# Kernel optimization log

Measured on AMD Instinct MI355X. Metric: run time of the kernel, lower is better.

The kernel has to match this reference:

```python
import jax, jax.numpy as jnp
import numpy as np

B, L, LATENT, HID, NTOK = 65536, 8, 256, 128, 5


def setup_inputs() -> dict:
    key = jax.random.key(0)
    ks = jax.random.split(key, 8)
    s = 0.05  # small init scale for stable GRU dynamics
    return {
        "latent_context": jax.random.normal(ks[0], (B, LATENT), jnp.float32),
        "target_sequence": jax.random.randint(ks[1], (B, L), 0, NTOK),
        "emb_table": jax.random.normal(ks[2], (NTOK + 1, HID), jnp.float32) * s,
        "W_ih": jax.random.normal(ks[3], (3 * LATENT, HID), jnp.float32) * s,
        "W_hh": jax.random.normal(ks[4], (3 * LATENT, LATENT), jnp.float32) * s,
        "b_ih": jnp.zeros((3 * LATENT,), jnp.float32),
        "b_hh": jnp.zeros((3 * LATENT,), jnp.float32),
        "W_out": jax.random.normal(ks[5], (NTOK, LATENT), jnp.float32) * s,
        "b_out": jnp.zeros((NTOK,), jnp.float32),
    }


def reference(latent_context, target_sequence, emb_table, W_ih, W_hh, b_ih, b_hh, W_out, b_out):
    b = latent_context.shape[0]
    start_idx = emb_table.shape[0] - 1  # start token index = num_tokens
    # Teacher forcing: input token at step 0 is <start>, then target[:, :-1]
    tokens = jnp.concatenate(
        [jnp.full((b, 1), start_idx, dtype=target_sequence.dtype), target_sequence[:, :-1]],
        axis=1,
    )  # (B, L)
    emb = emb_table[tokens]  # (B, L, HID) embedding gather, done once

    def gru_step(h, x):
        # x: (B, HID), h: (B, LATENT). PyTorch GRU cell math.
        gi = x @ W_ih.T + b_ih          # (B, 3*LATENT)
        gh = h @ W_hh.T + b_hh          # (B, 3*LATENT)
        i_r, i_z, i_n = jnp.split(gi, 3, axis=-1)
        h_r, h_z, h_n = jnp.split(gh, 3, axis=-1)
        r = jax.nn.sigmoid(i_r + h_r)
        z = jax.nn.sigmoid(i_z + h_z)
        n = jnp.tanh(i_n + r * h_n)
        h_new = (1.0 - z) * n + z * h
        step_logits = h_new @ W_out.T + b_out  # (B, NTOK)
        return h_new, step_logits

    _, logits = jax.lax.scan(gru_step, latent_context, jnp.swapaxes(emb, 0, 1))
    return jnp.swapaxes(logits, 0, 1)  # (B, L, NTOK)
```

## Files before the change

kernel.cpp:

```cpp
#include <hip/hip_runtime.h>
#include <hip/hip_bf16.h>


typedef __attribute__((ext_vector_type(8)))  __bf16 bf16x8;
typedef __attribute__((ext_vector_type(4)))  __bf16 bf16x4;
typedef __attribute__((ext_vector_type(8)))  unsigned short u16x8;
typedef __attribute__((ext_vector_type(4)))  float  f32x4;

#define LOG2E_F     1.4426950408889634f
#define TWO_LOG2E_F 2.8853900817779268f

#if __has_builtin(__builtin_amdgcn_exp2f)
#define EXP2F(x) __builtin_amdgcn_exp2f(x)
#else
#define EXP2F(x) __expf((x) * 0.6931471805599453f)
#endif

__device__ __forceinline__ float sigm2(float a) {
    return __builtin_amdgcn_rcpf(1.f + EXP2F(-a));
}
__device__ __forceinline__ float tanh2(float a) {
    return __builtin_fmaf(2.f, __builtin_amdgcn_rcpf(1.f + EXP2F(-a)), -1.f);
}
__device__ __forceinline__ void lds_barrier() {
    __builtin_amdgcn_sched_barrier(0);
    asm volatile("s_waitcnt lgkmcnt(0)" ::: "memory");
    __builtin_amdgcn_s_barrier();
    __builtin_amdgcn_sched_barrier(0);
}

#define MFMA16(a, b, c) __builtin_amdgcn_mfma_f32_16x16x32_bf16((a), (b), (c), 0, 0, 0)

__global__ void k_gtable(const float* __restrict__ emb, const float* __restrict__ W_ih,
                         const float* __restrict__ b_ih, const float* __restrict__ b_hh,
                         float* __restrict__ G) {
    int tok = blockIdx.x;
    int j   = threadIdx.x;
    const float4* e4 = (const float4*)(emb + tok * 128);
    const float4* w4 = (const float4*)(W_ih + (size_t)j * 128);
    float s = 0.f;
#pragma unroll
    for (int k = 0; k < 32; ++k) {
        float4 a = e4[k], b = w4[k];
        s += a.x * b.x + a.y * b.y + a.z * b.z + a.w * b.w;
    }
    s += b_ih[j];
    if (j < 512) s = (s + b_hh[j]) * LOG2E_F;
    else         s = s * TWO_LOG2E_F;
    G[tok * 768 + j] = s;
}

__global__ void k_wfrag3(const float* __restrict__ Whh, const float* __restrict__ Gtab,
                         const float* __restrict__ b_hh, __bf16* __restrict__ Wg) {
    int u    = blockIdx.x * 256 + threadIdx.x;
    int lane = u & 63;
    int frag = u >> 6;
    int w    = frag / 28;
    int f    = frag - 28 * w;
    int col  = w * 16 + (lane & 15);
    int kq   = lane >> 4;
    bf16x8 v;
    if (f < 24) {
        int g = f >> 3, kc = f & 7;
        float scale = (g < 2) ? LOG2E_F : TWO_LOG2E_F;
        const float* src = Whh + (size_t)(g * 256 + col) * 256 + kc * 32 + kq * 8;
#pragma unroll
        for (int j = 0; j < 8; ++j) v[j] = (__bf16)(src[j] * scale);
    } else {
        int g = f - 24;
#pragma unroll
        for (int j = 0; j < 8; ++j) {
            int k = kq * 8 + j;
            float val = 0.f;
            if (k < 6) {
                val = (g == 0) ? Gtab[k * 768 + col]
                    : (g == 1) ? Gtab[k * 768 + 256 + col]
                    : (g == 2) ? b_hh[512 + col] * TWO_LOG2E_F
                               : Gtab[k * 768 + 512 + col];
            }
            v[j] = (__bf16)val;
        }
    }
    *(bf16x8*)(Wg + (size_t)u * 8) = v;
}

__global__ __launch_bounds__(1024) void k_main(
    const float* __restrict__ latent, const int* __restrict__ tgt,
    const __bf16* __restrict__ Wg, const float* __restrict__ Wout,
    const float* __restrict__ bout, float* __restrict__ out) {

    __shared__ __bf16 h_lds[2][4][8][64][8];
    __shared__ __bf16 ohc_lds[8][4][16][8];
    __shared__ __bf16 wstage_lds[16][4][64][8];
    __shared__ __bf16 woutf_lds[8][64][8];
    __shared__ float  logit_lds[64 * 40];

    const int tid  = threadIdx.x;
    const int lane = tid & 63;
    const int w    = tid >> 6;
    const int q    = lane >> 4;
    const int n16  = lane & 15;
    const int row0 = blockIdx.x * 64;

    const __bf16* wbase = Wg + ((size_t)(w * 28) * 64 + lane) * 8;

    const int kc_h  = w >> 1;
    const int slotl = n16 + 16 * ((2 * w + (q >> 1)) & 3);
    const int joff  = 4 * (q & 1);

    if (tid < 512) {
        int kc = tid >> 6, ln = tid & 63, m = ln & 15, kq2 = ln >> 4;
        bf16x8 v;
#pragma unroll
        for (int j = 0; j < 8; ++j)
            v[j] = (m < 5) ? (__bf16)Wout[m * 256 + kc * 32 + kq2 * 8 + j] : (__bf16)0.f;
        *(bf16x8*)&woutf_lds[kc][ln][0] = v;
    }
    if (tid < 512) {
        int t = tid >> 6, nt = (tid >> 4) & 3, nn = tid & 15;
        int tok = (t == 0) ? 5 : tgt[(size_t)(row0 + nt * 16 + nn) * 8 + t - 1];
        u16x8 o;
#pragma unroll
        for (int j = 0; j < 8; ++j) o[j] = (j == tok) ? (unsigned short)0x3F80 : (unsigned short)0;
        *(u16x8*)&ohc_lds[t][nt][nn][0] = o;
    }
    for (int idx = tid; idx < 4096; idx += 1024) {
        int ws = idx >> 8, f = (idx >> 6) & 3, ln = idx & 63;
        bf16x8 v = *(const bf16x8*)(Wg + ((size_t)(ws * 28 + 24 + f) * 64 + ln) * 8);
        *(bf16x8*)&wstage_lds[ws][f][ln][0] = v;
    }
#pragma unroll
    for (int nt = 0; nt < 4; ++nt) {
        float4 hv = *(const float4*)(latent + (size_t)(row0 + nt * 16 + n16) * 256 + 16 * w + 4 * q);
        bf16x4 hb;
        hb[0] = (__bf16)hv.x; hb[1] = (__bf16)hv.y;
        hb[2] = (__bf16)hv.z; hb[3] = (__bf16)hv.w;
        *(bf16x4*)&h_lds[0][nt][kc_h][slotl][joff] = hb;
    }
    const int lw = (w == 0) ? 0 : (w == 5) ? 1 : (w == 10) ? 2 : (w == 15) ? 3 : -1;
    const float bo0 = bout[0], bo1 = bout[1], bo2 = bout[2], bo3 = bout[3], bo4 = bout[4];
    const f32x4 z4 = {0.f, 0.f, 0.f, 0.f};
    const bf16x8 zoh = __builtin_bit_cast(bf16x8, (u16x8){0, 0, 0, 0, 0, 0, 0, 0});
    __syncthreads();

    for (int t = 0; t < 8; ++t) {
        const int cur = t & 1, nxt = cur ^ 1;
        f32x4 acc[4][4];

        __builtin_amdgcn_s_setprio(1);
        {
            bf16x8 a0 = *(const bf16x8*)&wstage_lds[w][0][lane][0];
            bf16x8 a1 = *(const bf16x8*)&wstage_lds[w][1][lane][0];
            bf16x8 a2 = *(const bf16x8*)&wstage_lds[w][2][lane][0];
            bf16x8 a3 = *(const bf16x8*)&wstage_lds[w][3][lane][0];
#pragma unroll
            for (int nt = 0; nt < 4; ++nt) {
                bf16x8 ov = *(const bf16x8*)&ohc_lds[t][nt][n16][0];
                bf16x8 oh = (q == 0) ? ov : zoh;
                acc[0][nt] = MFMA16(a0, oh, z4);
                acc[1][nt] = MFMA16(a1, oh, z4);
                acc[2][nt] = MFMA16(a2, oh, z4);
                acc[3][nt] = MFMA16(a3, oh, z4);
            }
        }
#pragma unroll 2
        for (int kc = 0; kc < 8; ++kc) {
            bf16x8 a0 = *(const bf16x8*)(wbase + (size_t)kc * 512);
            bf16x8 a1 = *(const bf16x8*)(wbase + (size_t)(8 + kc) * 512);
            bf16x8 a2 = *(const bf16x8*)(wbase + (size_t)(16 + kc) * 512);
#pragma unroll
            for (int nt = 0; nt < 4; ++nt) {
                bf16x8 bb = *(const bf16x8*)&h_lds[cur][nt][kc][lane][0];
                acc[0][nt] = MFMA16(a0, bb, acc[0][nt]);
                acc[1][nt] = MFMA16(a1, bb, acc[1][nt]);
                acc[2][nt] = MFMA16(a2, bb, acc[2][nt]);
            }
        }

        if (lw >= 0 && t > 0) {
            f32x4 lacc = z4;
#pragma unroll
            for (int kc = 0; kc < 8; ++kc) {
                bf16x8 wf = *(const bf16x8*)&woutf_lds[kc][lane][0];
                bf16x8 bb = *(const bf16x8*)&h_lds[cur][lw][kc][lane][0];
                lacc = MFMA16(wf, bb, lacc);
            }
            float* dst = &logit_lds[(lw * 16 + n16) * 40 + (t - 1) * 5];
            if (q == 0) {
                dst[0] = lacc[0] + bo0; dst[1] = lacc[1] + bo1;
                dst[2] = lacc[2] + bo2; dst[3] = lacc[3] + bo3;
            } else if (q == 1) {
                dst[4] = lacc[0] + bo4;
            }
        }
        __builtin_amdgcn_s_setprio(0);

#pragma unroll
        for (int nt = 0; nt < 4; ++nt) {
            bf16x4 hold = *(const bf16x4*)&h_lds[cur][nt][kc_h][slotl][joff];
            bf16x4 hb;
#pragma unroll
            for (int i = 0; i < 4; ++i) {
                float rg = sigm2(acc[0][nt][i]);
                float zg = sigm2(acc[1][nt][i]);
                float ng = tanh2(__builtin_fmaf(rg, acc[2][nt][i], acc[3][nt][i]));
                float hv = ng + zg * ((float)hold[i] - ng);
                hb[i] = (__bf16)hv;
            }
            *(bf16x4*)&h_lds[nxt][nt][kc_h][slotl][joff] = hb;
        }
        lds_barrier();
    }

    if (lw >= 0) {
        f32x4 lacc = z4;
#pragma unroll
        for (int kc = 0; kc < 8; ++kc) {
            bf16x8 wf = *(const bf16x8*)&woutf_lds[kc][lane][0];
            bf16x8 bb = *(const bf16x8*)&h_lds[0][lw][kc][lane][0];
            lacc = MFMA16(wf, bb, lacc);
        }
        float* dst = &logit_lds[(lw * 16 + n16) * 40 + 7 * 5];
        if (q == 0) {
            dst[0] = lacc[0] + bo0; dst[1] = lacc[1] + bo1;
            dst[2] = lacc[2] + bo2; dst[3] = lacc[3] + bo3;
        } else if (q == 1) {
            dst[4] = lacc[0] + bo4;
        }
    }
    __syncthreads();
    for (int i = tid; i < 64 * 40; i += 1024)
        out[(size_t)row0 * 40 + i] = logit_lds[i];
}

extern "C" void kernel_launch(void* const* d_in, const int* in_sizes, int n_in,
                              void* d_out, int out_size, void* d_ws, size_t ws_size,
                              hipStream_t stream) {
    const float* latent = (const float*)d_in[0];
    const int*   tgt    = (const int*)d_in[1];
    const float* emb    = (const float*)d_in[2];
    const float* W_ih   = (const float*)d_in[3];
    const float* W_hh   = (const float*)d_in[4];
    const float* b_ih   = (const float*)d_in[5];
    const float* b_hh   = (const float*)d_in[6];
    const float* W_out  = (const float*)d_in[7];
    const float* b_out  = (const float*)d_in[8];
    float* out = (float*)d_out;

    float*  Gtab = (float*)d_ws;
    __bf16* Wg   = (__bf16*)((char*)d_ws + 18432);

    k_gtable<<<6, 768, 0, stream>>>(emb, W_ih, b_ih, b_hh, Gtab);
    k_wfrag3<<<112, 256, 0, stream>>>(W_hh, Gtab, b_hh, Wg);
    k_main<<<1024, 1024, 0, stream>>>(latent, tgt, Wg, W_out, b_out, out);
}
```

Before: 250.7 us.

## Stream GRU weights via global-to-LDS DMA double buffer with single h buffer

Each timestep now streams the recurrent weight fragments from global memory into per-wave LDS slots with global_load_lds, double-buffered and waited on with explicit vmcnt. Previously they were loaded into registers each timestep. The one-hot input-gate weights now stay in registers instead of an LDS stage. The h state drops from two LDS buffers to one, which needs an extra barrier before the in-place update. The aim is to overlap weight fetch with MFMA work and free LDS, at the cost of an extra barrier per step and hand-managed wait counts.

```diff
diff --git a/kernel.cpp b/kernel.cpp
--- a/kernel.cpp
+++ b/kernel.cpp
@@ -27,6 +27,11 @@
     asm volatile("s_waitcnt lgkmcnt(0)" ::: "memory");
     __builtin_amdgcn_s_barrier();
     __builtin_amdgcn_sched_barrier(0);
+}
+__device__ __forceinline__ void dma16(const __bf16* g, __bf16* l) {
+    __builtin_amdgcn_global_load_lds(
+        (const __attribute__((address_space(1))) unsigned int*)g,
+        (__attribute__((address_space(3))) unsigned int*)l, 16, 0, 0);
 }
 
 #define MFMA16(a, b, c) __builtin_amdgcn_mfma_f32_16x16x32_bf16((a), (b), (c), 0, 0, 0)
@@ -89,9 +94,9 @@
     const __bf16* __restrict__ Wg, const float* __restrict__ Wout,
     const float* __restrict__ bout, float* __restrict__ out) {
 
-    __shared__ __bf16 h_lds[2][4][8][64][8];
+    __shared__ __bf16 h_lds[4][8][64][8];
+    __shared__ __bf16 wst[16][2][3][64][8];
     __shared__ __bf16 ohc_lds[8][4][16][8];
-    __shared__ __bf16 wstage_lds[16][4][64][8];
     __shared__ __bf16 woutf_lds[8][64][8];
     __shared__ float  logit_lds[64 * 40];
 
@@ -103,6 +108,8 @@
     const int row0 = blockIdx.x * 64;
 
     const __bf16* wbase = Wg + ((size_t)(w * 28) * 64 + lane) * 8;
+    __bf16* slot0 = &wst[w][0][0][0][0];
+    __bf16* slot1 = &wst[w][1][0][0][0];
 
     const int kc_h  = w >> 1;
     const int slotl = n16 + 16 * ((2 * w + (q >> 1)) & 3);
@@ -123,11 +130,6 @@
 #pragma unroll
         for (int j = 0; j < 8; ++j) o[j] = (j == tok) ? (unsigned short)0x3F80 : (unsigned short)0;
         *(u16x8*)&ohc_lds[t][nt][nn][0] = o;
-    }
-    for (int idx = tid; idx < 4096; idx += 1024) {
-        int ws = idx >> 8, f = (idx >> 6) & 3, ln = idx & 63;
-        bf16x8 v = *(const bf16x8*)(Wg + ((size_t)(ws * 28 + 24 + f) * 64 + ln) * 8);
-        *(bf16x8*)&wstage_lds[ws][f][ln][0] = v;
     }
 #pragma unroll
     for (int nt = 0; nt < 4; ++nt) {
@@ -135,54 +137,87 @@
         bf16x4 hb;
         hb[0] = (__bf16)hv.x; hb[1] = (__bf16)hv.y;
         hb[2] = (__bf16)hv.z; hb[3] = (__bf16)hv.w;
-        *(bf16x4*)&h_lds[0][nt][kc_h][slotl][joff] = hb;
-    }
+        *(bf16x4*)&h_lds[nt][kc_h][slotl][joff] = hb;
+    }
+    bf16x8 ohA0 = *(const bf16x8*)(wbase + (size_t)24 * 512);
+    bf16x8 ohA1 = *(const bf16x8*)(wbase + (size_t)25 * 512);
+    bf16x8 ohA2 = *(const bf16x8*)(wbase + (size_t)26 * 512);
+    bf16x8 ohA3 = *(const bf16x8*)(wbase + (size_t)27 * 512);
+
     const int lw = (w == 0) ? 0 : (w == 5) ? 1 : (w == 10) ? 2 : (w == 15) ? 3 : -1;
     const float bo0 = bout[0], bo1 = bout[1], bo2 = bout[2], bo3 = bout[3], bo4 = bout[4];
     const f32x4 z4 = {0.f, 0.f, 0.f, 0.f};
     const bf16x8 zoh = __builtin_bit_cast(bf16x8, (u16x8){0, 0, 0, 0, 0, 0, 0, 0});
+
     __syncthreads();
 
+#define DMA_GRP(kc_, sptr)                                            \
+    dma16(wbase + (size_t)(kc_)*512,        (sptr) + 0 * 512);        \
+    dma16(wbase + (size_t)(8 + (kc_))*512,  (sptr) + 1 * 512);        \
+    dma16(wbase + (size_t)(16 + (kc_))*512, (sptr) + 2 * 512);
+
+    DMA_GRP(0, slot0)
+    DMA_GRP(1, slot1)
+
+#define GROUP(i_, sptr, WN, FIRST)                                    \
+    {                                                                 \
+        asm volatile("s_waitcnt vmcnt(" WN ")" ::: "memory");         \
+        __builtin_amdgcn_sched_barrier(0);                            \
+        bf16x8 a0 = *(const bf16x8*)((sptr) + 0 * 512 + lane * 8);    \
+        bf16x8 a1 = *(const bf16x8*)((sptr) + 1 * 512 + lane * 8);    \
+        bf16x8 a2 = *(const bf16x8*)((sptr) + 2 * 512 + lane * 8);    \
+        bf16x8 b0 = *(const bf16x8*)&h_lds[0][i_][lane][0];           \
+        bf16x8 b1 = *(const bf16x8*)&h_lds[1][i_][lane][0];           \
+        bf16x8 b2 = *(const bf16x8*)&h_lds[2][i_][lane][0];           \
+        bf16x8 b3 = *(const bf16x8*)&h_lds[3][i_][lane][0];           \
+        asm volatile("s_waitcnt lgkmcnt(0)" ::: "memory");            \
+        __builtin_amdgcn_sched_barrier(0);                            \
+        if ((i_) < 6) { DMA_GRP((i_) + 2, sptr) }                     \
+        if (FIRST) {                                                  \
+            acc0[0] = MFMA16(a0, b0, z4); acc0[1] = MFMA16(a0, b1, z4); \
+            acc0[2] = MFMA16(a0, b2, z4); acc0[3] = MFMA16(a0, b3, z4); \
+            acc1[0] = MFMA16(a1, b0, z4); acc1[1] = MFMA16(a1, b1, z4); \
+            acc1[2] = MFMA16(a1, b2, z4); acc1[3] = MFMA16(a1, b3, z4); \
+            acc2[0] = MFMA16(a2, b0, z4); acc2[1] = MFMA16(a2, b1, z4); \
+            acc2[2] = MFMA16(a2, b2, z4); acc2[3] = MFMA16(a2, b3, z4); \
+        } else {                                                      \
+            acc0[0] = MFMA16(a0, b0, acc0[0]); acc0[1] = MFMA16(a0, b1, acc0[1]); \
+            acc0[2] = MFMA16(a0, b2, acc0[2]); acc0[3] = MFMA16(a0, b3, acc0[3]); \
+            acc1[0] = MFMA16(a1, b0, acc1[0]); acc1[1] = MFMA16(a1, b1, acc1[1]); \
+            acc1[2] = MFMA16(a1, b2, acc1[2]); acc1[3] = MFMA16(a1, b3, acc1[3]); \
+            acc2[0] = MFMA16(a2, b0, acc2[0]); acc2[1] = MFMA16(a2, b1, acc2[1]); \
+            acc2[2] = MFMA16(a2, b2, acc2[2]); acc2[3] = MFMA16(a2, b3, acc2[3]); \
+        }                                                             \
+    }
+
     for (int t = 0; t < 8; ++t) {
-        const int cur = t & 1, nxt = cur ^ 1;
-        f32x4 acc[4][4];
+        f32x4 acc0[4], acc1[4], acc2[4], acc3[4];
 
         __builtin_amdgcn_s_setprio(1);
-        {
-            bf16x8 a0 = *(const bf16x8*)&wstage_lds[w][0][lane][0];
-            bf16x8 a1 = *(const bf16x8*)&wstage_lds[w][1][lane][0];
-            bf16x8 a2 = *(const bf16x8*)&wstage_lds[w][2][lane][0];
-            bf16x8 a3 = *(const bf16x8*)&wstage_lds[w][3][lane][0];
-#pragma unroll
-            for (int nt = 0; nt < 4; ++nt) {
-                bf16x8 ov = *(const bf16x8*)&ohc_lds[t][nt][n16][0];
-                bf16x8 oh = (q == 0) ? ov : zoh;
-                acc[0][nt] = MFMA16(a0, oh, z4);
-                acc[1][nt] = MFMA16(a1, oh, z4);
-                acc[2][nt] = MFMA16(a2, oh, z4);
-                acc[3][nt] = MFMA16(a3, oh, z4);
-            }
-        }
-#pragma unroll 2
-        for (int kc = 0; kc < 8; ++kc) {
-            bf16x8 a0 = *(const bf16x8*)(wbase + (size_t)kc * 512);
-            bf16x8 a1 = *(const bf16x8*)(wbase + (size_t)(8 + kc) * 512);
-            bf16x8 a2 = *(const bf16x8*)(wbase + (size_t)(16 + kc) * 512);
-#pragma unroll
-            for (int nt = 0; nt < 4; ++nt) {
-                bf16x8 bb = *(const bf16x8*)&h_lds[cur][nt][kc][lane][0];
-                acc[0][nt] = MFMA16(a0, bb, acc[0][nt]);
-                acc[1][nt] = MFMA16(a1, bb, acc[1][nt]);
-                acc[2][nt] = MFMA16(a2, bb, acc[2][nt]);
-            }
-        }
-
+        GROUP(0, slot0, "3", 1)
+        GROUP(1, slot1, "3", 0)
+        GROUP(2, slot0, "3", 0)
+        GROUP(3, slot1, "3", 0)
+        GROUP(4, slot0, "3", 0)
+        GROUP(5, slot1, "3", 0)
+        GROUP(6, slot0, "3", 0)
+        GROUP(7, slot1, "0", 0)
+
+#pragma unroll
+        for (int nt = 0; nt < 4; ++nt) {
+            bf16x8 ov = *(const bf16x8*)&ohc_lds[t][nt][n16][0];
+            bf16x8 oh = (q == 0) ? ov : zoh;
+            acc0[nt] = MFMA16(ohA0, oh, acc0[nt]);
+            acc1[nt] = MFMA16(ohA1, oh, acc1[nt]);
+            acc2[nt] = MFMA16(ohA2, oh, acc2[nt]);
+            acc3[nt] = MFMA16(ohA3, oh, z4);
+        }
         if (lw >= 0 && t > 0) {
             f32x4 lacc = z4;
 #pragma unroll
             for (int kc = 0; kc < 8; ++kc) {
                 bf16x8 wf = *(const bf16x8*)&woutf_lds[kc][lane][0];
-                bf16x8 bb = *(const bf16x8*)&h_lds[cur][lw][kc][lane][0];
+                bf16x8 bb = *(const bf16x8*)&h_lds[lw][kc][lane][0];
                 lacc = MFMA16(wf, bb, lacc);
             }
             float* dst = &logit_lds[(lw * 16 + n16) * 40 + (t - 1) * 5];
@@ -195,19 +230,26 @@
         }
         __builtin_amdgcn_s_setprio(0);
 
+        lds_barrier();
+
 #pragma unroll
         for (int nt = 0; nt < 4; ++nt) {
-            bf16x4 hold = *(const bf16x4*)&h_lds[cur][nt][kc_h][slotl][joff];
+            bf16x4* hp = (bf16x4*)&h_lds[nt][kc_h][slotl][joff];
+            bf16x4 hold = *hp;
             bf16x4 hb;
 #pragma unroll
             for (int i = 0; i < 4; ++i) {
-                float rg = sigm2(acc[0][nt][i]);
-                float zg = sigm2(acc[1][nt][i]);
-                float ng = tanh2(__builtin_fmaf(rg, acc[2][nt][i], acc[3][nt][i]));
+                float rg = sigm2(acc0[nt][i]);
+                float zg = sigm2(acc1[nt][i]);
+                float ng = tanh2(__builtin_fmaf(rg, acc2[nt][i], acc3[nt][i]));
                 float hv = ng + zg * ((float)hold[i] - ng);
                 hb[i] = (__bf16)hv;
             }
-            *(bf16x4*)&h_lds[nxt][nt][kc_h][slotl][joff] = hb;
+            *hp = hb;
+        }
+        if (t < 7) {
+            DMA_GRP(0, slot0)
+            DMA_GRP(1, slot1)
         }
         lds_barrier();
     }
@@ -217,7 +259,7 @@
 #pragma unroll
         for (int kc = 0; kc < 8; ++kc) {
             bf16x8 wf = *(const bf16x8*)&woutf_lds[kc][lane][0];
-            bf16x8 bb = *(const bf16x8*)&h_lds[0][lw][kc][lane][0];
+            bf16x8 bb = *(const bf16x8*)&h_lds[lw][kc][lane][0];
             lacc = MFMA16(wf, bb, lacc);
         }
         float* dst = &logit_lds[(lw * 16 + n16) * 40 + 7 * 5];
@@ -231,6 +273,8 @@
     __syncthreads();
     for (int i = tid; i < 64 * 40; i += 1024)
         out[(size_t)row0 * 40 + i] = logit_lds[i];
+#undef GROUP
+#undef DMA_GRP
 }
 
 extern "C" void kernel_launch(void* const* d_in, const int* in_sizes, int n_in,
```

After: 440.9 us. +75.9%, slower.
